# Optimization experiments

Measured on AMD Instinct MI355X. Metric: run time of the kernel, lower is better.

## Reference

```python
import jax, jax.numpy as jnp
import numpy as np

PRO_NUM, MAX_LEN, HID = 64, 1024, 256
TERM_NUM = 512


def setup_inputs() -> dict:
    key = jax.random.key(0)
    k1, k2, k3 = jax.random.split(key, 3)
    term_encoding = jax.random.normal(k1, (TERM_NUM, HID), dtype=jnp.float32)
    pro_encoding = jax.random.normal(k2, (PRO_NUM, MAX_LEN, HID), dtype=jnp.float32)
    # lengths in [1, MAX_LEN] so no row is fully masked (avoids NaN softmax)
    pro_lens = jax.random.randint(k3, (PRO_NUM,), 1, MAX_LEN + 1)
    return {"term_encoding": term_encoding, "pro_encoding": pro_encoding, "pro_lens": pro_lens}


def reference(term_encoding, pro_encoding, pro_lens):
    # scores: pro_num x term_num x max_len  (QK^T without sqrt(d) scaling, as in original)
    scores = jnp.einsum("plh,th->ptl", pro_encoding, term_encoding)
    max_len = pro_encoding.shape[1]
    # mask positions >= pro_lens (per protein), broadcast over term dim
    mask = jnp.arange(max_len)[None, None, :] >= pro_lens[:, None, None]  # p,1,l
    scores = jnp.where(mask, -jnp.inf, scores)
    attn = jax.nn.softmax(scores, axis=-1)  # pro_num x term_num x max_len
    out = jnp.einsum("ptl,plh->pth", attn, pro_encoding)  # pro_num x term_num x hid
    return (out, attn)
```

## Files before the change

### kernel.cpp

```cpp
#include <hip/hip_runtime.h>

#define PRO_NUM 64
#define TERM_NUM 512
#define MAX_LEN 1024
#define HID 256

typedef _Float16 f16x8 __attribute__((ext_vector_type(8)));
typedef _Float16 f16x4 __attribute__((ext_vector_type(4)));
typedef float f32x4 __attribute__((ext_vector_type(4)));


__device__ __forceinline__ f16x8 cvt8(const float* __restrict__ s) {
  float4 a = *(const float4*)s;
  float4 b = *(const float4*)(s + 4);
  f16x8 r = {(_Float16)a.x, (_Float16)a.y, (_Float16)a.z, (_Float16)a.w,
             (_Float16)b.x, (_Float16)b.y, (_Float16)b.z, (_Float16)b.w};
  return r;
}

__global__ __launch_bounds__(256) void k_prep(const float* __restrict__ pro,
                                              f16x8* __restrict__ fragP,
                                              f16x8* __restrict__ fragT) {
  __shared__ _Float16 ldsA[64][264];
  const int p = blockIdx.y;
  const int lc = blockIdx.x;
  const int tid = threadIdx.x;

  const float* src = pro + ((size_t)p * MAX_LEN + lc * 64) * HID;
  #pragma unroll
  for (int j = 0; j < 16; ++j) {
    int idx = j * 1024 + tid * 4;
    int l = idx >> 8, h = idx & 255;
    float4 v = *(const float4*)(src + idx);
    ldsA[l][h + 0] = (_Float16)v.x;
    ldsA[l][h + 1] = (_Float16)v.y;
    ldsA[l][h + 2] = (_Float16)v.z;
    ldsA[l][h + 3] = (_Float16)v.w;
  }
  __syncthreads();

  const int w = tid >> 6;
  const int lane = tid & 63;
  const int lr = lane & 15;
  const int lg = lane >> 4;

  {
    const int T = lc * 4 + w;
    f16x8* dst = fragP + ((size_t)(p * 64 + T) * 8) * 64 + lane;
    #pragma unroll
    for (int kk = 0; kk < 8; ++kk)
      dst[kk * 64] = *(const f16x8*)&ldsA[w * 16 + lr][kk * 32 + lg * 8];
  }
  #pragma unroll
  for (int hh = 0; hh < 4; ++hh) {
    const int H = w * 4 + hh;
    #pragma unroll
    for (int k2 = 0; k2 < 2; ++k2) {
      const int kc = lc * 2 + k2;
      const int lloc = k2 * 32 + lg * 8;
      f16x8 v;
      #pragma unroll
      for (int i = 0; i < 8; ++i) v[i] = ldsA[lloc + i][H * 16 + lr];
      fragT[((size_t)(p * 16 + H) * 32 + kc) * 64 + lane] = v;
    }
  }
}

__global__ __launch_bounds__(256) void k_fused(
    const float* __restrict__ term, const f16x8* __restrict__ fragP,
    const f16x8* __restrict__ fragT, const int* __restrict__ lens,
    float* __restrict__ attn, float* __restrict__ out) {
  __shared__ __align__(16) _Float16 attn_lds[32][1024];
  __shared__ float rmx[4][32];
  __shared__ float rsm[4][32];

  const int bid = blockIdx.x;
  const int swz = (bid & 7) * 128 + (bid >> 3);
  const int p = swz >> 4;
  const int t0 = (swz & 15) * 32;

  const int tid = threadIdx.x;
  const int w = tid >> 6;
  const int lane = tid & 63;
  const int lr = lane & 15;
  const int lg = lane >> 4;
  const int len = lens[p];
  const int l0w = w * 256;

  f32x4 acc[2][16];
  #pragma unroll
  for (int mt = 0; mt < 2; ++mt)
    #pragma unroll
    for (int i = 0; i < 16; ++i) acc[mt][i] = (f32x4){0.f, 0.f, 0.f, 0.f};

  const float* trow0 = term + (size_t)(t0 + lr) * HID + lg * 8;
  const f16x8* pbw = fragP + ((size_t)(p * 64 + w * 16) * 8) * 64 + lane;

  #pragma unroll
  for (int kk = 0; kk < 8; ++kk) {
    f16x8 a0 = cvt8(trow0 + kk * 32);
    f16x8 a1 = cvt8(trow0 + (size_t)16 * HID + kk * 32);
    f16x8 bf[16];
    #pragma unroll
    for (int tile = 0; tile < 16; ++tile) bf[tile] = pbw[(tile * 8 + kk) * 64];
    #pragma unroll
    for (int tile = 0; tile < 16; ++tile) {
      acc[0][tile] = __builtin_amdgcn_mfma_f32_16x16x32_f16(a0, bf[tile], acc[0][tile], 0, 0, 0);
      acc[1][tile] = __builtin_amdgcn_mfma_f32_16x16x32_f16(a1, bf[tile], acc[1][tile], 0, 0, 0);
    }
  }

  float rmax[2][4];
  #pragma unroll
  for (int mt = 0; mt < 2; ++mt)
    #pragma unroll
    for (int r = 0; r < 4; ++r) rmax[mt][r] = -INFINITY;

  #pragma unroll
  for (int tile = 0; tile < 16; ++tile) {
    int l = l0w + tile * 16 + lr;
    #pragma unroll
    for (int mt = 0; mt < 2; ++mt) {
      #pragma unroll
      for (int r = 0; r < 4; ++r) {
        float s = (l < len) ? acc[mt][tile][r] : -INFINITY;
        acc[mt][tile][r] = s;
        rmax[mt][r] = fmaxf(rmax[mt][r], s);
      }
    }
  }
  #pragma unroll
  for (int m = 1; m < 16; m <<= 1) {
    #pragma unroll
    for (int mt = 0; mt < 2; ++mt)
      #pragma unroll
      for (int r = 0; r < 4; ++r) rmax[mt][r] = fmaxf(rmax[mt][r], __shfl_xor(rmax[mt][r], m));
  }
  if (lr == 0) {
    #pragma unroll
    for (int mt = 0; mt < 2; ++mt)
      #pragma unroll
      for (int r = 0; r < 4; ++r) rmx[w][mt * 16 + lg * 4 + r] = rmax[mt][r];
  }
  __syncthreads();
  float fm[2][4];
  #pragma unroll
  for (int mt = 0; mt < 2; ++mt)
    #pragma unroll
    for (int r = 0; r < 4; ++r) {
      int row = mt * 16 + lg * 4 + r;
      fm[mt][r] = fmaxf(fmaxf(rmx[0][row], rmx[1][row]), fmaxf(rmx[2][row], rmx[3][row]));
    }

  float rsum[2][4] = {{0.f, 0.f, 0.f, 0.f}, {0.f, 0.f, 0.f, 0.f}};
  #pragma unroll
  for (int tile = 0; tile < 16; ++tile) {
    #pragma unroll
    for (int mt = 0; mt < 2; ++mt) {
      #pragma unroll
      for (int r = 0; r < 4; ++r) {
        float e = __expf(acc[mt][tile][r] - fm[mt][r]);
        acc[mt][tile][r] = e;
        rsum[mt][r] += e;
      }
    }
  }
  #pragma unroll
  for (int m = 1; m < 16; m <<= 1) {
    #pragma unroll
    for (int mt = 0; mt < 2; ++mt)
      #pragma unroll
      for (int r = 0; r < 4; ++r) rsum[mt][r] += __shfl_xor(rsum[mt][r], m);
  }
  if (lr == 0) {
    #pragma unroll
    for (int mt = 0; mt < 2; ++mt)
      #pragma unroll
      for (int r = 0; r < 4; ++r) rsm[w][mt * 16 + lg * 4 + r] = rsum[mt][r];
  }
  __syncthreads();
  float inv[2][4];
  #pragma unroll
  for (int mt = 0; mt < 2; ++mt)
    #pragma unroll
    for (int r = 0; r < 4; ++r) {
      int row = mt * 16 + lg * 4 + r;
      inv[mt][r] = 1.0f / (rsm[0][row] + rsm[1][row] + rsm[2][row] + rsm[3][row]);
    }

  #pragma unroll
  for (int mt = 0; mt < 2; ++mt) {
    #pragma unroll
    for (int r = 0; r < 4; ++r) {
      const int row = mt * 16 + lg * 4 + r;
      float* arow = attn + ((size_t)(p * TERM_NUM + t0 + row)) * MAX_LEN + l0w + lr;
      const int sw = (row & 7) << 3;
      #pragma unroll
      for (int tile = 0; tile < 16; ++tile) {
        float v = acc[mt][tile][r] * inv[mt][r];
        arow[tile * 16] = v;
        attn_lds[row][(l0w + tile * 16 + lr) ^ sw] = (_Float16)v;
      }
    }
  }
  __syncthreads();

  f32x4 acc2[2][4];
  #pragma unroll
  for (int mt = 0; mt < 2; ++mt)
    #pragma unroll
    for (int nt = 0; nt < 4; ++nt) acc2[mt][nt] = (f32x4){0.f, 0.f, 0.f, 0.f};

  const f16x8* btw = fragT + ((size_t)(p * 16 + w * 4) * 32) * 64 + lane;
  const int kcmax = (len + 31) >> 5;

  #pragma unroll 4
  for (int kc = 0; kc < kcmax; ++kc) {
    const int k0 = kc * 32;
    f16x8 a[2];
    #pragma unroll
    for (int mt = 0; mt < 2; ++mt) {
      const int row = mt * 16 + lr;
      a[mt] = *(const f16x8*)&attn_lds[row][(k0 + lg * 8) ^ ((row & 7) << 3)];
    }
    #pragma unroll
    for (int nt = 0; nt < 4; ++nt) {
      f16x8 bf = btw[(nt * 32 + kc) * 64];
      acc2[0][nt] = __builtin_amdgcn_mfma_f32_16x16x32_f16(a[0], bf, acc2[0][nt], 0, 0, 0);
      acc2[1][nt] = __builtin_amdgcn_mfma_f32_16x16x32_f16(a[1], bf, acc2[1][nt], 0, 0, 0);
    }
  }

  #pragma unroll
  for (int mt = 0; mt < 2; ++mt) {
    #pragma unroll
    for (int nt = 0; nt < 4; ++nt) {
      #pragma unroll
      for (int r = 0; r < 4; ++r) {
        out[((size_t)p * TERM_NUM + t0 + mt * 16 + lg * 4 + r) * HID + w * 64 + nt * 16 + lr] =
            acc2[mt][nt][r];
      }
    }
  }
}

extern "C" void kernel_launch(void* const* d_in, const int* in_sizes, int n_in,
                              void* d_out, int out_size, void* d_ws, size_t ws_size,
                              hipStream_t stream) {
  const float* term = (const float*)d_in[0];
  const float* pro  = (const float*)d_in[1];
  const int*   lens = (const int*)d_in[2];

  float* out  = (float*)d_out;
  float* attn = out + (size_t)PRO_NUM * TERM_NUM * HID;

  f16x8* fragP = (f16x8*)d_ws;
  f16x8* fragT = fragP + (size_t)PRO_NUM * 64 * 8 * 64;

  k_prep<<<dim3(MAX_LEN / 64, PRO_NUM), 256, 0, stream>>>(pro, fragP, fragT);
  k_fused<<<dim3(PRO_NUM * (TERM_NUM / 32)), 256, 0, stream>>>(term, fragP, fragT, lens, attn, out);
}
```

Measured before the change: 135.9 us.

## Halve term tile per block and write attn via LDS with vectorized stores

Each block now handles 16 terms instead of 32, doubling the grid and halving accumulator registers and LDS. Launch bounds ask for 4 waves per SIMD. The attention output is staged through LDS and written with contiguous float4 stores instead of strided scalar stores. The LDS staging means attn values are rounded through fp16 before being written to global memory, which lowers output precision. Each block also reloads the protein fragments for half as many terms, which doubles fragP traffic.

```diff
diff --git a/kernel.cpp b/kernel.cpp
--- a/kernel.cpp
+++ b/kernel.cpp
@@ -66,18 +66,18 @@
   }
 }
 
-__global__ __launch_bounds__(256) void k_fused(
+__global__ __launch_bounds__(256, 4) void k_fused(
     const float* __restrict__ term, const f16x8* __restrict__ fragP,
     const f16x8* __restrict__ fragT, const int* __restrict__ lens,
     float* __restrict__ attn, float* __restrict__ out) {
-  __shared__ __align__(16) _Float16 attn_lds[32][1024];
-  __shared__ float rmx[4][32];
-  __shared__ float rsm[4][32];
+  __shared__ __align__(16) _Float16 attn_lds[16][1024];
+  __shared__ float rmx[4][16];
+  __shared__ float rsm[4][16];
 
   const int bid = blockIdx.x;
-  const int swz = (bid & 7) * 128 + (bid >> 3);
-  const int p = swz >> 4;
-  const int t0 = (swz & 15) * 32;
+  const int swz = (bid & 7) * 256 + (bid >> 3);
+  const int p = swz >> 5;
+  const int t0 = (swz & 31) * 16;
 
   const int tid = threadIdx.x;
   const int w = tid >> 6;
@@ -87,11 +87,9 @@
   const int len = lens[p];
   const int l0w = w * 256;
 
-  f32x4 acc[2][16];
-  #pragma unroll
-  for (int mt = 0; mt < 2; ++mt)
-    #pragma unroll
-    for (int i = 0; i < 16; ++i) acc[mt][i] = (f32x4){0.f, 0.f, 0.f, 0.f};
+  f32x4 acc[16];
+  #pragma unroll
+  for (int i = 0; i < 16; ++i) acc[i] = (f32x4){0.f, 0.f, 0.f, 0.f};
 
   const float* trow0 = term + (size_t)(t0 + lr) * HID + lg * 8;
   const f16x8* pbw = fragP + ((size_t)(p * 64 + w * 16) * 8) * 64 + lane;
@@ -99,117 +97,106 @@
   #pragma unroll
   for (int kk = 0; kk < 8; ++kk) {
     f16x8 a0 = cvt8(trow0 + kk * 32);
-    f16x8 a1 = cvt8(trow0 + (size_t)16 * HID + kk * 32);
-    f16x8 bf[16];
-    #pragma unroll
-    for (int tile = 0; tile < 16; ++tile) bf[tile] = pbw[(tile * 8 + kk) * 64];
-    #pragma unroll
-    for (int tile = 0; tile < 16; ++tile) {
-      acc[0][tile] = __builtin_amdgcn_mfma_f32_16x16x32_f16(a0, bf[tile], acc[0][tile], 0, 0, 0);
-      acc[1][tile] = __builtin_amdgcn_mfma_f32_16x16x32_f16(a1, bf[tile], acc[1][tile], 0, 0, 0);
-    }
-  }
-
-  float rmax[2][4];
-  #pragma unroll
-  for (int mt = 0; mt < 2; ++mt)
-    #pragma unroll
-    for (int r = 0; r < 4; ++r) rmax[mt][r] = -INFINITY;
-
+    #pragma unroll
+    for (int g = 0; g < 4; ++g) {
+      f16x8 bf[4];
+      #pragma unroll
+      for (int t = 0; t < 4; ++t) bf[t] = pbw[((g * 4 + t) * 8 + kk) * 64];
+      #pragma unroll
+      for (int t = 0; t < 4; ++t)
+        acc[g * 4 + t] = __builtin_amdgcn_mfma_f32_16x16x32_f16(a0, bf[t], acc[g * 4 + t], 0, 0, 0);
+    }
+  }
+
+  float rmax[4] = {-INFINITY, -INFINITY, -INFINITY, -INFINITY};
   #pragma unroll
   for (int tile = 0; tile < 16; ++tile) {
     int l = l0w + tile * 16 + lr;
     #pragma unroll
-    for (int mt = 0; mt < 2; ++mt) {
-      #pragma unroll
-      for (int r = 0; r < 4; ++r) {
-        float s = (l < len) ? acc[mt][tile][r] : -INFINITY;
-        acc[mt][tile][r] = s;
-        rmax[mt][r] = fmaxf(rmax[mt][r], s);
-      }
+    for (int r = 0; r < 4; ++r) {
+      float s = (l < len) ? acc[tile][r] : -INFINITY;
+      acc[tile][r] = s;
+      rmax[r] = fmaxf(rmax[r], s);
     }
   }
   #pragma unroll
   for (int m = 1; m < 16; m <<= 1) {
     #pragma unroll
-    for (int mt = 0; mt < 2; ++mt)
-      #pragma unroll
-      for (int r = 0; r < 4; ++r) rmax[mt][r] = fmaxf(rmax[mt][r], __shfl_xor(rmax[mt][r], m));
+    for (int r = 0; r < 4; ++r) rmax[r] = fmaxf(rmax[r], __shfl_xor(rmax[r], m));
   }
   if (lr == 0) {
     #pragma unroll
-    for (int mt = 0; mt < 2; ++mt)
-      #pragma unroll
-      for (int r = 0; r < 4; ++r) rmx[w][mt * 16 + lg * 4 + r] = rmax[mt][r];
-  }
-  __syncthreads();
-  float fm[2][4];
-  #pragma unroll
-  for (int mt = 0; mt < 2; ++mt)
+    for (int r = 0; r < 4; ++r) rmx[w][lg * 4 + r] = rmax[r];
+  }
+  __syncthreads();
+  float fm[4];
+  #pragma unroll
+  for (int r = 0; r < 4; ++r) {
+    int row = lg * 4 + r;
+    fm[r] = fmaxf(fmaxf(rmx[0][row], rmx[1][row]), fmaxf(rmx[2][row], rmx[3][row]));
+  }
+  float rsum[4] = {0.f, 0.f, 0.f, 0.f};
+  #pragma unroll
+  for (int tile = 0; tile < 16; ++tile) {
     #pragma unroll
     for (int r = 0; r < 4; ++r) {
-      int row = mt * 16 + lg * 4 + r;
-      fm[mt][r] = fmaxf(fmaxf(rmx[0][row], rmx[1][row]), fmaxf(rmx[2][row], rmx[3][row]));
-    }
-
-  float rsum[2][4] = {{0.f, 0.f, 0.f, 0.f}, {0.f, 0.f, 0.f, 0.f}};
-  #pragma unroll
-  for (int tile = 0; tile < 16; ++tile) {
-    #pragma unroll
-    for (int mt = 0; mt < 2; ++mt) {
-      #pragma unroll
-      for (int r = 0; r < 4; ++r) {
-        float e = __expf(acc[mt][tile][r] - fm[mt][r]);
-        acc[mt][tile][r] = e;
-        rsum[mt][r] += e;
-      }
+      float e = __expf(acc[tile][r] - fm[r]);
+      acc[tile][r] = e;
+      rsum[r] += e;
     }
   }
   #pragma unroll
   for (int m = 1; m < 16; m <<= 1) {
     #pragma unroll
-    for (int mt = 0; mt < 2; ++mt)
-      #pragma unroll
-      for (int r = 0; r < 4; ++r) rsum[mt][r] += __shfl_xor(rsum[mt][r], m);
+    for (int r = 0; r < 4; ++r) rsum[r] += __shfl_xor(rsum[r], m);
   }
   if (lr == 0) {
     #pragma unroll
-    for (int mt = 0; mt < 2; ++mt)
-      #pragma unroll
-      for (int r = 0; r < 4; ++r) rsm[w][mt * 16 + lg * 4 + r] = rsum[mt][r];
-  }
-  __syncthreads();
-  float inv[2][4];
-  #pragma unroll
-  for (int mt = 0; mt < 2; ++mt)
-    #pragma unroll
-    for (int r = 0; r < 4; ++r) {
-      int row = mt * 16 + lg * 4 + r;
-      inv[mt][r] = 1.0f / (rsm[0][row] + rsm[1][row] + rsm[2][row] + rsm[3][row]);
-    }
-
-  #pragma unroll
-  for (int mt = 0; mt < 2; ++mt) {
-    #pragma unroll
-    for (int r = 0; r < 4; ++r) {
-      const int row = mt * 16 + lg * 4 + r;
-      float* arow = attn + ((size_t)(p * TERM_NUM + t0 + row)) * MAX_LEN + l0w + lr;
-      const int sw = (row & 7) << 3;
-      #pragma unroll
-      for (int tile = 0; tile < 16; ++tile) {
-        float v = acc[mt][tile][r] * inv[mt][r];
-        arow[tile * 16] = v;
-        attn_lds[row][(l0w + tile * 16 + lr) ^ sw] = (_Float16)v;
-      }
-    }
-  }
-  __syncthreads();
-
-  f32x4 acc2[2][4];
-  #pragma unroll
-  for (int mt = 0; mt < 2; ++mt)
-    #pragma unroll
-    for (int nt = 0; nt < 4; ++nt) acc2[mt][nt] = (f32x4){0.f, 0.f, 0.f, 0.f};
+    for (int r = 0; r < 4; ++r) rsm[w][lg * 4 + r] = rsum[r];
+  }
+  __syncthreads();
+  float inv[4];
+  #pragma unroll
+  for (int r = 0; r < 4; ++r) {
+    int row = lg * 4 + r;
+    inv[r] = 1.0f / (rsm[0][row] + rsm[1][row] + rsm[2][row] + rsm[3][row]);
+  }
+
+  #pragma unroll
+  for (int r = 0; r < 4; ++r) {
+    const int row = lg * 4 + r;
+    const int sw = (row & 7) << 3;
+    #pragma unroll
+    for (int tile = 0; tile < 16; ++tile) {
+      attn_lds[row][(l0w + tile * 16 + lr) ^ sw] = (_Float16)(acc[tile][r] * inv[r]);
+    }
+  }
+  __syncthreads();
+
+  {
+    const int row = w * 4 + lg;
+    const int sw = (row & 7) << 3;
+    float* arow = attn + ((size_t)(p * TERM_NUM + t0 + row)) * MAX_LEN;
+    #pragma unroll
+    for (int j = 0; j < 4; ++j) {
+      const int c0 = j * 256 + lr * 16;
+      f16x8 v0 = *(const f16x8*)&attn_lds[row][c0 ^ sw];
+      f16x8 v1 = *(const f16x8*)&attn_lds[row][(c0 + 8) ^ sw];
+      float4 o;
+      o = (float4){(float)v0[0], (float)v0[1], (float)v0[2], (float)v0[3]};
+      *(float4*)(arow + c0 + 0) = o;
+      o = (float4){(float)v0[4], (float)v0[5], (float)v0[6], (float)v0[7]};
+      *(float4*)(arow + c0 + 4) = o;
+      o = (float4){(float)v1[0], (float)v1[1], (float)v1[2], (float)v1[3]};
+      *(float4*)(arow + c0 + 8) = o;
+      o = (float4){(float)v1[4], (float)v1[5], (float)v1[6], (float)v1[7]};
+      *(float4*)(arow + c0 + 12) = o;
+    }
+  }
+
+  f32x4 acc2[4];
+  #pragma unroll
+  for (int nt = 0; nt < 4; ++nt) acc2[nt] = (f32x4){0.f, 0.f, 0.f, 0.f};
 
   const f16x8* btw = fragT + ((size_t)(p * 16 + w * 4) * 32) * 64 + lane;
   const int kcmax = (len + 31) >> 5;
@@ -217,29 +204,20 @@
   #pragma unroll 4
   for (int kc = 0; kc < kcmax; ++kc) {
     const int k0 = kc * 32;
-    f16x8 a[2];
-    #pragma unroll
-    for (int mt = 0; mt < 2; ++mt) {
-      const int row = mt * 16 + lr;
-      a[mt] = *(const f16x8*)&attn_lds[row][(k0 + lg * 8) ^ ((row & 7) << 3)];
-    }
+    const int row = lr;
+    f16x8 a = *(const f16x8*)&attn_lds[row][(k0 + lg * 8) ^ ((row & 7) << 3)];
     #pragma unroll
     for (int nt = 0; nt < 4; ++nt) {
       f16x8 bf = btw[(nt * 32 + kc) * 64];
-      acc2[0][nt] = __builtin_amdgcn_mfma_f32_16x16x32_f16(a[0], bf, acc2[0][nt], 0, 0, 0);
-      acc2[1][nt] = __builtin_amdgcn_mfma_f32_16x16x32_f16(a[1], bf, acc2[1][nt], 0, 0, 0);
-    }
-  }
-
-  #pragma unroll
-  for (int mt = 0; mt < 2; ++mt) {
-    #pragma unroll
-    for (int nt = 0; nt < 4; ++nt) {
-      #pragma unroll
-      for (int r = 0; r < 4; ++r) {
-        out[((size_t)p * TERM_NUM + t0 + mt * 16 + lg * 4 + r) * HID + w * 64 + nt * 16 + lr] =
-            acc2[mt][nt][r];
-      }
+      acc2[nt] = __builtin_amdgcn_mfma_f32_16x16x32_f16(a, bf, acc2[nt], 0, 0, 0);
+    }
+  }
+
+  #pragma unroll
+  for (int nt = 0; nt < 4; ++nt) {
+    #pragma unroll
+    for (int r = 0; r < 4; ++r) {
+      out[((size_t)p * TERM_NUM + t0 + lg * 4 + r) * HID + w * 64 + nt * 16 + lr] = acc2[nt][r];
     }
   }
 }
@@ -258,5 +236,5 @@
   f16x8* fragT = fragP + (size_t)PRO_NUM * 64 * 8 * 64;
 
   k_prep<<<dim3(MAX_LEN / 64, PRO_NUM), 256, 0, stream>>>(pro, fragP, fragT);
-  k_fused<<<dim3(PRO_NUM * (TERM_NUM / 32)), 256, 0, stream>>>(term, fragP, fragT, lens, attn, out);
-}
+  k_fused<<<dim3(PRO_NUM * (TERM_NUM / 16)), 256, 0, stream>>>(term, fragP, fragT, lens, attn, out);
+}
```

Measured after the change: 172.3 us. 1.27x slower.
